# Optimization experiments

Measured on AMD Instinct MI355X. Metric: run time of the kernel, lower is better.

Reference implementation:

```python
import jax, jax.numpy as jnp
import numpy as np

N, S, T, E, H = 4, 2048, 2048, 512, 8
HD = E // H  # head_dim = 64


def setup_inputs() -> dict:
    key0 = jax.random.key(0)
    ks = jax.random.split(key0, 12)
    sc = 1.0 / np.sqrt(E)
    inp = {
        "query": jax.random.normal(ks[0], (N, S, E), jnp.float32),
        "key": jax.random.normal(ks[1], (N, T, E), jnp.float32),
        "value": jax.random.normal(ks[2], (N, T, E), jnp.float32),
        "attn_mask": jnp.tril(jnp.ones((S, T), jnp.int32)),  # causal: 0 => masked
        # nn.Linear weights (out, in) and biases, torch convention y = x @ W.T + b
        "Wq": jax.random.normal(ks[3], (E, E), jnp.float32) * sc,
        "bq": jax.random.normal(ks[4], (E,), jnp.float32) * sc,
        "Wk": jax.random.normal(ks[5], (E, E), jnp.float32) * sc,
        "bk": jax.random.normal(ks[6], (E,), jnp.float32) * sc,
        "Wv": jax.random.normal(ks[7], (E, E), jnp.float32) * sc,
        "bv": jax.random.normal(ks[8], (E,), jnp.float32) * sc,
        "Wp": jax.random.normal(ks[9], (E, E), jnp.float32) * sc,
        "bp": jax.random.normal(ks[10], (E,), jnp.float32) * sc,
    }
    return inp


def reference(query, key, value, attn_mask, Wq, bq, Wk, bk, Wv, bv, Wp, bp):
    # QKV projections, split heads: (N, H, L, HD)
    q = (query @ Wq.T + bq).reshape(N, S, H, HD).transpose(0, 2, 1, 3)
    k = (key @ Wk.T + bk).reshape(N, T, H, HD).transpose(0, 2, 1, 3)
    v = (value @ Wv.T + bv).reshape(N, T, H, HD).transpose(0, 2, 1, 3)
    # scaled scores (N, H, S, T) -- intentionally materialized like the original
    e = jnp.einsum("nhsd,nhtd->nhst", q, k) / jnp.sqrt(jnp.float32(HD))
    e = jnp.where(attn_mask == 0, -jnp.inf, e)
    a = jax.nn.softmax(e, axis=-1)
    # dropout is identity in eval mode (reference runs deterministic/eval)
    y = jnp.einsum("nhst,nhtd->nhsd", a, v)
    y = y.transpose(0, 2, 1, 3).reshape(N, S, E)
    return y @ Wp.T + bp
```

## Files before the change

kernel.cpp:

```cpp
#include <hip/hip_runtime.h>


#define DEV __device__ __forceinline__

typedef unsigned short u16;
typedef unsigned int u32;
typedef __bf16 bf16x8 __attribute__((ext_vector_type(8)));
typedef float f32x4 __attribute__((ext_vector_type(4)));

#define MFMA_BF16(A, B, C) __builtin_amdgcn_mfma_f32_16x16x32_bf16(A, B, C, 0, 0, 0)

DEV u16 f2bf(float f) {
  u32 u = __builtin_bit_cast(u32, f);
  u += 0x7fffu + ((u >> 16) & 1u);
  return (u16)(u >> 16);
}
DEV u16 f2bf_ru(float f) {
  u32 u = __builtin_bit_cast(u32, f);
  return (u16)((u + 0x8000u) >> 16);
}

DEV void cp16(void* l, const void* g) {
  __builtin_amdgcn_global_load_lds(
      (const __attribute__((address_space(1))) u32*)g,
      (__attribute__((address_space(3))) u32*)l, 16, 0, 0);
}

__global__ __launch_bounds__(256) void cast3(const float* __restrict__ q,
                                             const float* __restrict__ k,
                                             const float* __restrict__ v,
                                             u16* qo, u16* ko, u16* vo) {
  const float* s = (blockIdx.y == 0) ? q : (blockIdx.y == 1) ? k : v;
  u16* d = (blockIdx.y == 0) ? qo : (blockIdx.y == 1) ? ko : vo;
  int i = blockIdx.x * 256 + threadIdx.x;
  float4 f = ((const float4*)s)[i];
  ushort4 o;
  o.x = f2bf(f.x); o.y = f2bf(f.y); o.z = f2bf(f.z); o.w = f2bf(f.w);
  ((ushort4*)d)[i] = o;
}

__global__ __launch_bounds__(256) void cast4(const float* __restrict__ a,
                                             const float* __restrict__ b,
                                             const float* __restrict__ c,
                                             const float* __restrict__ d2,
                                             u16* ao, u16* bo, u16* co, u16* do_) {
  int y = blockIdx.y;
  const float* s = (y == 0) ? a : (y == 1) ? b : (y == 2) ? c : d2;
  u16* d = (y == 0) ? ao : (y == 1) ? bo : (y == 2) ? co : do_;
  int i = blockIdx.x * 256 + threadIdx.x;
  float4 f = ((const float4*)s)[i];
  ushort4 o;
  o.x = f2bf(f.x); o.y = f2bf(f.y); o.z = f2bf(f.z); o.w = f2bf(f.w);
  ((ushort4*)d)[i] = o;
}

DEV void gemm_loop(const u16* __restrict__ A, const u16* __restrict__ W,
                   u16* As, u16* Bs, int m0, int n0, int tid, f32x4 acc[4][4]) {
  const int lane = tid & 63, wid = tid >> 6;
  const int wm = wid & 1, wn = wid >> 1;
  const int l15 = lane & 15, l4 = lane >> 4;
  for (int kt = 0; kt < 512; kt += 32) {
    __syncthreads();
#pragma unroll
    for (int i = 0; i < 2; ++i) {
      int c = tid + 256 * i;
      int row = c >> 2, kc = (c & 3) * 8;
      cp16(&As[c * 8], A + (m0 + row) * 512 + kt + kc);
      cp16(&Bs[c * 8], W + (n0 + row) * 512 + kt + kc);
    }
    __syncthreads();
    bf16x8 af[4], bfr[4];
#pragma unroll
    for (int f = 0; f < 4; ++f) {
      af[f]  = *(const bf16x8*)&As[(wm * 64 + f * 16 + l15) * 32 + l4 * 8];
      bfr[f] = *(const bf16x8*)&Bs[(wn * 64 + f * 16 + l15) * 32 + l4 * 8];
    }
#pragma unroll
    for (int fm = 0; fm < 4; ++fm)
#pragma unroll
      for (int fn = 0; fn < 4; ++fn)
        acc[fm][fn] = MFMA_BF16(af[fm], bfr[fn], acc[fm][fn]);
  }
}

__global__ __launch_bounds__(256) void gemm_qkv(
    const u16* __restrict__ qx, const u16* __restrict__ kx, const u16* __restrict__ vx,
    const u16* __restrict__ wq, const u16* __restrict__ wk, const u16* __restrict__ wv,
    const float* __restrict__ bq, const float* __restrict__ bk, const float* __restrict__ bv,
    u16* qp, u16* kp, u16* vp) {
  __shared__ u16 As[128 * 32];
  __shared__ u16 Bs[128 * 32];
  const int wsel = blockIdx.x >> 2;
  const u16* A = (wsel == 0) ? qx : (wsel == 1) ? kx : vx;
  const u16* W = (wsel == 0) ? wq : (wsel == 1) ? wk : wv;
  const float* bias = (wsel == 0) ? bq : (wsel == 1) ? bk : bv;
  u16* C = (wsel == 0) ? qp : (wsel == 1) ? kp : vp;
  const int n0 = (blockIdx.x & 3) * 128, m0 = blockIdx.y * 128;
  const int tid = threadIdx.x, lane = tid & 63, wid = tid >> 6;
  const int wm = wid & 1, wn = wid >> 1;
  const int l15 = lane & 15, l4 = lane >> 4;

  f32x4 acc[4][4] = {};
  gemm_loop(A, W, As, Bs, m0, n0, tid, acc);

#pragma unroll
  for (int fn = 0; fn < 4; ++fn) {
    int col = n0 + wn * 64 + fn * 16 + l15;
    float bvv = bias[col];
#pragma unroll
    for (int fm = 0; fm < 4; ++fm) {
      int rowb = m0 + wm * 64 + fm * 16 + l4 * 4;
#pragma unroll
      for (int r = 0; r < 4; ++r)
        C[(rowb + r) * 512 + col] = f2bf(acc[fm][fn][r] + bvv);
    }
  }
}

__global__ __launch_bounds__(256) void gemm_out(const u16* __restrict__ A,
                                                const u16* __restrict__ W,
                                                const float* __restrict__ bias,
                                                float* __restrict__ C) {
  __shared__ u16 As[128 * 32];
  __shared__ u16 Bs[128 * 32];
  const int n0 = blockIdx.x * 128, m0 = blockIdx.y * 128;
  const int tid = threadIdx.x, lane = tid & 63, wid = tid >> 6;
  const int wm = wid & 1, wn = wid >> 1;
  const int l15 = lane & 15, l4 = lane >> 4;

  f32x4 acc[4][4] = {};
  gemm_loop(A, W, As, Bs, m0, n0, tid, acc);

#pragma unroll
  for (int fn = 0; fn < 4; ++fn) {
    int col = n0 + wn * 64 + fn * 16 + l15;
    float bvv = bias[col];
#pragma unroll
    for (int fm = 0; fm < 4; ++fm) {
      int rowb = m0 + wm * 64 + fm * 16 + l4 * 4;
#pragma unroll
      for (int r = 0; r < 4; ++r)
        C[(rowb + r) * 512 + col] = acc[fm][fn][r] + bvv;
    }
  }
}

__global__ __launch_bounds__(256) void transpose_v(const u16* __restrict__ vp,
                                                   u16* __restrict__ vt) {
  __shared__ u16 L[64 * 72];
  const int bid = blockIdx.x;
  const int nh = bid & 31, tt = bid >> 5;
  const int n = nh >> 3, h = nh & 7;
  const u16* src = vp + (n * 2048 + tt * 64) * 512 + h * 64;
  const int tid = threadIdx.x;
#pragma unroll
  for (int i = 0; i < 2; ++i) {
    int c = tid + 256 * i;
    int row = c >> 3, dg = c & 7;
    uint4 x = *(const uint4*)(src + row * 512 + dg * 8);
    *(uint4*)&L[row * 72 + dg * 8] = x;
  }
  __syncthreads();
  u16* dst = vt + nh * 64 * 2048 + tt * 64;
#pragma unroll
  for (int i = 0; i < 2; ++i) {
    int c = tid + 256 * i;
    int d = c >> 3, tg = c & 7;
    u16 e[8];
#pragma unroll
    for (int j = 0; j < 8; ++j) e[j] = L[(tg * 8 + j) * 72 + d];
    uint4 o;
    o.x = (u32)e[0] | ((u32)e[1] << 16);
    o.y = (u32)e[2] | ((u32)e[3] << 16);
    o.z = (u32)e[4] | ((u32)e[5] << 16);
    o.w = (u32)e[6] | ((u32)e[7] << 16);
    *(uint4*)(dst + d * 2048 + tg * 8) = o;
  }
}

__global__ __launch_bounds__(256) void attn_kernel(const u16* __restrict__ Qg,
                                                   const u16* __restrict__ Kg,
                                                   const u16* __restrict__ Vt,
                                                   u16* __restrict__ Yg) {
  __shared__ u16 Qs[64 * 64];
  __shared__ u16 KP[64 * 136];
  __shared__ u16 Vts[64 * 128];

  const int bid = blockIdx.x;
  const int nh = bid & 31;
  const int qt = 31 - (bid >> 5);
  const int n = nh >> 3, h = nh & 7;
  const int tid = threadIdx.x, lane = tid & 63, w = tid >> 6;
  const int l15 = lane & 15, l4 = lane >> 4;
  const int s0 = qt * 64;

  const u16* Qb = Qg + (n * 2048 + s0) * 512 + h * 64;
  const u16* Kb = Kg + n * 2048 * 512 + h * 64;
  const u16* Vb = Vt + nh * 64 * 2048;

#pragma unroll
  for (int i = 0; i < 2; ++i) {
    int c = tid + 256 * i;
    int row = c >> 3, dg = (c & 7) ^ (row & 7);
    cp16(&Qs[c * 8], Qb + row * 512 + dg * 8);
  }
  __syncthreads();
  const int qr = w * 16 + l15;
  bf16x8 qf0 = *(const bf16x8*)&Qs[qr * 64 + ((l4 ^ (qr & 7)) * 8)];
  bf16x8 qf1 = *(const bf16x8*)&Qs[qr * 64 + (((4 + l4) ^ (qr & 7)) * 8)];

  f32x4 accO[4] = {};
  float mrow = -1e30f, lrow = 0.f;
  const int sgl = s0 + w * 16 + l15;

  const int ntiles = (qt >> 1) + 1;
  for (int it = 0; it < ntiles; ++it) {
    const int t0 = it * 128;
    __syncthreads();
#pragma unroll
    for (int i = 0; i < 4; ++i) {
      int c = tid + 256 * i;
      int t = c >> 3, dg = (c & 7) ^ (t & 7);
      cp16(&KP[c * 8], Kb + (t0 + t) * 512 + dg * 8);
    }
#pragma unroll
    for (int i = 0; i < 4; ++i) {
      int c = tid + 256 * i;
      int d = c >> 4, tgs = c & 15;
      cp16(&Vts[c * 8], Vb + d * 2048 + t0 + ((tgs ^ (d & 15)) * 8));
    }
    __syncthreads();

    f32x4 st[8];
#pragma unroll
    for (int fn = 0; fn < 8; ++fn) {
      int tr = fn * 16 + l15;
      bf16x8 k0 = *(const bf16x8*)&KP[tr * 64 + ((l4 ^ (tr & 7)) * 8)];
      bf16x8 k1 = *(const bf16x8*)&KP[tr * 64 + (((4 + l4) ^ (tr & 7)) * 8)];
      f32x4 a = {};
      a = MFMA_BF16(k0, qf0, a);
      st[fn] = MFMA_BF16(k1, qf1, a);
    }

    const bool diag = (t0 + 128 > s0);
    const float SC = 0.18033688f;
    float rmax = -1e30f;
#pragma unroll
    for (int fn = 0; fn < 8; ++fn)
#pragma unroll
      for (int r = 0; r < 4; ++r) {
        float v = st[fn][r] * SC;
        if (diag) {
          int tg = t0 + fn * 16 + l4 * 4 + r;
          if (tg > sgl) v = -1e30f;
        }
        st[fn][r] = v;
        rmax = fmaxf(rmax, v);
      }
    rmax = fmaxf(rmax, __shfl_xor(rmax, 16));
    rmax = fmaxf(rmax, __shfl_xor(rmax, 32));
    float mnew = fmaxf(mrow, rmax);
    float alpha = __builtin_amdgcn_exp2f(mrow - mnew);
    mrow = mnew;
    float rsum = 0.f;
#pragma unroll
    for (int fn = 0; fn < 8; ++fn)
#pragma unroll
      for (int r = 0; r < 4; ++r) {
        float p = __builtin_amdgcn_exp2f(st[fn][r] - mnew);
        st[fn][r] = p;
        rsum += p;
      }
    rsum += __shfl_xor(rsum, 16);
    rsum += __shfl_xor(rsum, 32);
    lrow = lrow * alpha + rsum;

    float aO[4];
#pragma unroll
    for (int r = 0; r < 4; ++r) aO[r] = __shfl(alpha, (lane & 48) | (l4 * 4 + r));
#pragma unroll
    for (int fd = 0; fd < 4; ++fd)
#pragma unroll
      for (int r = 0; r < 4; ++r) accO[fd][r] *= aO[r];

    __syncthreads();

#pragma unroll
    for (int fn = 0; fn < 8; ++fn) {
      ushort4 pk;
      pk.x = f2bf_ru(st[fn][0]);
      pk.y = f2bf_ru(st[fn][1]);
      pk.z = f2bf_ru(st[fn][2]);
      pk.w = f2bf_ru(st[fn][3]);
      *(ushort4*)&KP[(w * 16 + l15) * 136 + fn * 16 + l4 * 4] = pk;
    }

#pragma unroll
    for (int ks = 0; ks < 4; ++ks) {
      bf16x8 ap = *(const bf16x8*)&KP[(w * 16 + l15) * 136 + ks * 32 + l4 * 8];
#pragma unroll
      for (int fd = 0; fd < 4; ++fd) {
        int d = fd * 16 + l15;
        bf16x8 bv = *(const bf16x8*)&Vts[d * 128 + (((ks * 4 + l4) ^ (d & 15)) * 8)];
        accO[fd] = MFMA_BF16(ap, bv, accO[fd]);
      }
    }
  }

  float lO[4];
#pragma unroll
  for (int r = 0; r < 4; ++r) lO[r] = __shfl(lrow, (lane & 48) | (l4 * 4 + r));
#pragma unroll
  for (int fd = 0; fd < 4; ++fd)
#pragma unroll
    for (int r = 0; r < 4; ++r) {
      int row = s0 + w * 16 + l4 * 4 + r;
      int col = h * 64 + fd * 16 + l15;
      Yg[(n * 2048 + row) * 512 + col] = f2bf(accO[fd][r] / lO[r]);
    }
}

extern "C" void kernel_launch(void* const* d_in, const int* in_sizes, int n_in,
                              void* d_out, int out_size, void* d_ws, size_t ws_size,
                              hipStream_t stream) {
  (void)in_sizes; (void)n_in; (void)out_size; (void)ws_size;
  const float* query = (const float*)d_in[0];
  const float* key_  = (const float*)d_in[1];
  const float* value = (const float*)d_in[2];
  const float* Wq = (const float*)d_in[4];
  const float* bq = (const float*)d_in[5];
  const float* Wk = (const float*)d_in[6];
  const float* bk = (const float*)d_in[7];
  const float* Wv = (const float*)d_in[8];
  const float* bv = (const float*)d_in[9];
  const float* Wp = (const float*)d_in[10];
  const float* bp = (const float*)d_in[11];

  char* ws = (char*)d_ws;
  u16* qx  = (u16*)(ws);
  u16* kx  = (u16*)(ws + 8388608);
  u16* vx  = (u16*)(ws + 16777216);
  u16* wqx = (u16*)(ws + 25165824);
  u16* wkx = (u16*)(ws + 25690112);
  u16* wvx = (u16*)(ws + 26214400);
  u16* wpx = (u16*)(ws + 26738688);
  u16* qp  = (u16*)(ws + 27262976);
  u16* kp  = (u16*)(ws + 35651584);
  u16* vp  = (u16*)(ws + 44040192);
  u16* y   = qx;
  u16* vt  = kx;

  cast3<<<dim3(4096, 3), 256, 0, stream>>>(query, key_, value, qx, kx, vx);
  cast4<<<dim3(256, 4), 256, 0, stream>>>(Wq, Wk, Wv, Wp, wqx, wkx, wvx, wpx);

  gemm_qkv<<<dim3(12, 64), 256, 0, stream>>>(qx, kx, vx, wqx, wkx, wvx,
                                             bq, bk, bv, qp, kp, vp);
  transpose_v<<<1024, 256, 0, stream>>>(vp, vt);
  attn_kernel<<<1024, 256, 0, stream>>>(qp, kp, vt, y);
  gemm_out<<<dim3(4, 64), 256, 0, stream>>>(y, wpx, bp, (float*)d_out);
}
```

Baseline: 209.0 us.

## Keep P in registers, fold softmax scale into Q, lazy rescale, retile out GEMM

Folds the softmax scale into the Q projection epilogue, removes the LDS round-trip for the probability tile by converting S accumulators directly into MFMA A operands with matching V reads, and skips the output rescale unless the running max grows by more than a threshold. It also adds s_setprio around MFMA blocks and halves the gemm_out M tile to double its grid. The aim is to cut LDS traffic, a barrier, and per-tile rescale ALU work, and to give the output GEMM more blocks. The lazy rescale lets exponentials exceed 1 by up to 2^10, which relies on fp32 and bf16 range.

```diff
diff --git a/kernel.cpp b/kernel.cpp
--- a/kernel.cpp
+++ b/kernel.cpp
@@ -7,6 +7,7 @@
 typedef unsigned int u32;
 typedef __bf16 bf16x8 __attribute__((ext_vector_type(8)));
 typedef float f32x4 __attribute__((ext_vector_type(4)));
+typedef u32 u32x4 __attribute__((ext_vector_type(4)));
 
 #define MFMA_BF16(A, B, C) __builtin_amdgcn_mfma_f32_16x16x32_bf16(A, B, C, 0, 0, 0)
 
@@ -14,10 +15,6 @@
   u32 u = __builtin_bit_cast(u32, f);
   u += 0x7fffu + ((u >> 16) & 1u);
   return (u16)(u >> 16);
-}
-DEV u16 f2bf_ru(float f) {
-  u32 u = __builtin_bit_cast(u32, f);
-  return (u16)((u + 0x8000u) >> 16);
 }
 
 DEV void cp16(void* l, const void* g) {
@@ -99,6 +96,7 @@
   const int tid = threadIdx.x, lane = tid & 63, wid = tid >> 6;
   const int wm = wid & 1, wn = wid >> 1;
   const int l15 = lane & 15, l4 = lane >> 4;
+  const float osc = (wsel == 0) ? 0.18033688f : 1.0f;
 
   f32x4 acc[4][4] = {};
   gemm_loop(A, W, As, Bs, m0, n0, tid, acc);
@@ -112,7 +110,7 @@
       int rowb = m0 + wm * 64 + fm * 16 + l4 * 4;
 #pragma unroll
       for (int r = 0; r < 4; ++r)
-        C[(rowb + r) * 512 + col] = f2bf(acc[fm][fn][r] + bvv);
+        C[(rowb + r) * 512 + col] = f2bf((acc[fm][fn][r] + bvv) * osc);
     }
   }
 }
@@ -121,23 +119,48 @@
                                                 const u16* __restrict__ W,
                                                 const float* __restrict__ bias,
                                                 float* __restrict__ C) {
-  __shared__ u16 As[128 * 32];
+  __shared__ u16 As[64 * 32];
   __shared__ u16 Bs[128 * 32];
-  const int n0 = blockIdx.x * 128, m0 = blockIdx.y * 128;
+  const int n0 = blockIdx.x * 128, m0 = blockIdx.y * 64;
   const int tid = threadIdx.x, lane = tid & 63, wid = tid >> 6;
   const int wm = wid & 1, wn = wid >> 1;
   const int l15 = lane & 15, l4 = lane >> 4;
 
-  f32x4 acc[4][4] = {};
-  gemm_loop(A, W, As, Bs, m0, n0, tid, acc);
+  f32x4 acc[2][4] = {};
+  for (int kt = 0; kt < 512; kt += 32) {
+    __syncthreads();
+    {
+      int row = tid >> 2, kc = (tid & 3) * 8;
+      cp16(&As[tid * 8], A + (m0 + row) * 512 + kt + kc);
+    }
+#pragma unroll
+    for (int i = 0; i < 2; ++i) {
+      int c = tid + 256 * i;
+      int row = c >> 2, kc = (c & 3) * 8;
+      cp16(&Bs[c * 8], W + (n0 + row) * 512 + kt + kc);
+    }
+    __syncthreads();
+    bf16x8 af[2], bfr[4];
+#pragma unroll
+    for (int f = 0; f < 2; ++f)
+      af[f] = *(const bf16x8*)&As[(wm * 32 + f * 16 + l15) * 32 + l4 * 8];
+#pragma unroll
+    for (int f = 0; f < 4; ++f)
+      bfr[f] = *(const bf16x8*)&Bs[(wn * 64 + f * 16 + l15) * 32 + l4 * 8];
+#pragma unroll
+    for (int fm = 0; fm < 2; ++fm)
+#pragma unroll
+      for (int fn = 0; fn < 4; ++fn)
+        acc[fm][fn] = MFMA_BF16(af[fm], bfr[fn], acc[fm][fn]);
+  }
 
 #pragma unroll
   for (int fn = 0; fn < 4; ++fn) {
     int col = n0 + wn * 64 + fn * 16 + l15;
     float bvv = bias[col];
 #pragma unroll
-    for (int fm = 0; fm < 4; ++fm) {
-      int rowb = m0 + wm * 64 + fm * 16 + l4 * 4;
+    for (int fm = 0; fm < 2; ++fm) {
+      int rowb = m0 + wm * 32 + fm * 16 + l4 * 4;
 #pragma unroll
       for (int r = 0; r < 4; ++r)
         C[(rowb + r) * 512 + col] = acc[fm][fn][r] + bvv;
@@ -183,7 +206,7 @@
                                                    const u16* __restrict__ Vt,
                                                    u16* __restrict__ Yg) {
   __shared__ u16 Qs[64 * 64];
-  __shared__ u16 KP[64 * 136];
+  __shared__ u16 Ks[128 * 64];
   __shared__ u16 Vts[64 * 128];
 
   const int bid = blockIdx.x;
@@ -221,7 +244,7 @@
     for (int i = 0; i < 4; ++i) {
       int c = tid + 256 * i;
       int t = c >> 3, dg = (c & 7) ^ (t & 7);
-      cp16(&KP[c * 8], Kb + (t0 + t) * 512 + dg * 8);
+      cp16(&Ks[c * 8], Kb + (t0 + t) * 512 + dg * 8);
     }
 #pragma unroll
     for (int i = 0; i < 4; ++i) {
@@ -232,24 +255,25 @@
     __syncthreads();
 
     f32x4 st[8];
+    __builtin_amdgcn_s_setprio(1);
 #pragma unroll
     for (int fn = 0; fn < 8; ++fn) {
       int tr = fn * 16 + l15;
-      bf16x8 k0 = *(const bf16x8*)&KP[tr * 64 + ((l4 ^ (tr & 7)) * 8)];
-      bf16x8 k1 = *(const bf16x8*)&KP[tr * 64 + (((4 + l4) ^ (tr & 7)) * 8)];
+      bf16x8 k0 = *(const bf16x8*)&Ks[tr * 64 + ((l4 ^ (tr & 7)) * 8)];
+      bf16x8 k1 = *(const bf16x8*)&Ks[tr * 64 + (((4 + l4) ^ (tr & 7)) * 8)];
       f32x4 a = {};
       a = MFMA_BF16(k0, qf0, a);
       st[fn] = MFMA_BF16(k1, qf1, a);
     }
+    __builtin_amdgcn_s_setprio(0);
 
     const bool diag = (t0 + 128 > s0);
-    const float SC = 0.18033688f;
     float rmax = -1e30f;
 #pragma unroll
     for (int fn = 0; fn < 8; ++fn)
 #pragma unroll
       for (int r = 0; r < 4; ++r) {
-        float v = st[fn][r] * SC;
+        float v = st[fn][r];
         if (diag) {
           int tg = t0 + fn * 16 + l4 * 4 + r;
           if (tg > sgl) v = -1e30f;
@@ -259,52 +283,57 @@
       }
     rmax = fmaxf(rmax, __shfl_xor(rmax, 16));
     rmax = fmaxf(rmax, __shfl_xor(rmax, 32));
-    float mnew = fmaxf(mrow, rmax);
-    float alpha = __builtin_amdgcn_exp2f(mrow - mnew);
-    mrow = mnew;
+    if (__any(rmax > mrow + 10.f)) {
+      float mnew = fmaxf(mrow, rmax);
+      float alpha = __builtin_amdgcn_exp2f(mrow - mnew);
+      mrow = mnew;
+      lrow *= alpha;
+      float aO[4];
+#pragma unroll
+      for (int r = 0; r < 4; ++r) aO[r] = __shfl(alpha, (lane & 48) | (l4 * 4 + r));
+#pragma unroll
+      for (int fd = 0; fd < 4; ++fd)
+#pragma unroll
+        for (int r = 0; r < 4; ++r) accO[fd][r] *= aO[r];
+    }
     float rsum = 0.f;
 #pragma unroll
     for (int fn = 0; fn < 8; ++fn)
 #pragma unroll
       for (int r = 0; r < 4; ++r) {
-        float p = __builtin_amdgcn_exp2f(st[fn][r] - mnew);
+        float p = __builtin_amdgcn_exp2f(st[fn][r] - mrow);
         st[fn][r] = p;
         rsum += p;
       }
     rsum += __shfl_xor(rsum, 16);
     rsum += __shfl_xor(rsum, 32);
-    lrow = lrow * alpha + rsum;
-
-    float aO[4];
-#pragma unroll
-    for (int r = 0; r < 4; ++r) aO[r] = __shfl(alpha, (lane & 48) | (l4 * 4 + r));
-#pragma unroll
-    for (int fd = 0; fd < 4; ++fd)
-#pragma unroll
-      for (int r = 0; r < 4; ++r) accO[fd][r] *= aO[r];
-
-    __syncthreads();
-
-#pragma unroll
-    for (int fn = 0; fn < 8; ++fn) {
-      ushort4 pk;
-      pk.x = f2bf_ru(st[fn][0]);
-      pk.y = f2bf_ru(st[fn][1]);
-      pk.z = f2bf_ru(st[fn][2]);
-      pk.w = f2bf_ru(st[fn][3]);
-      *(ushort4*)&KP[(w * 16 + l15) * 136 + fn * 16 + l4 * 4] = pk;
-    }
-
+    lrow += rsum;
+
+    bf16x8 pa[4];
 #pragma unroll
     for (int ks = 0; ks < 4; ++ks) {
-      bf16x8 ap = *(const bf16x8*)&KP[(w * 16 + l15) * 136 + ks * 32 + l4 * 8];
+      bf16x8 t;
+      t[0] = (__bf16)st[2 * ks][0];     t[1] = (__bf16)st[2 * ks][1];
+      t[2] = (__bf16)st[2 * ks][2];     t[3] = (__bf16)st[2 * ks][3];
+      t[4] = (__bf16)st[2 * ks + 1][0]; t[5] = (__bf16)st[2 * ks + 1][1];
+      t[6] = (__bf16)st[2 * ks + 1][2]; t[7] = (__bf16)st[2 * ks + 1][3];
+      pa[ks] = t;
+    }
+
+    __builtin_amdgcn_s_setprio(1);
+#pragma unroll
+    for (int ks = 0; ks < 4; ++ks) {
 #pragma unroll
       for (int fd = 0; fd < 4; ++fd) {
         int d = fd * 16 + l15;
-        bf16x8 bv = *(const bf16x8*)&Vts[d * 128 + (((ks * 4 + l4) ^ (d & 15)) * 8)];
-        accO[fd] = MFMA_BF16(ap, bv, accO[fd]);
+        const u16* vrow = &Vts[d * 128];
+        uint2 v0 = *(const uint2*)&vrow[(((ks * 4 + (l4 >> 1)) ^ l15) * 8) + (l4 & 1) * 4];
+        uint2 v1 = *(const uint2*)&vrow[(((ks * 4 + 2 + (l4 >> 1)) ^ l15) * 8) + (l4 & 1) * 4];
+        u32x4 bw; bw.x = v0.x; bw.y = v0.y; bw.z = v1.x; bw.w = v1.y;
+        accO[fd] = MFMA_BF16(pa[ks], __builtin_bit_cast(bf16x8, bw), accO[fd]);
       }
     }
+    __builtin_amdgcn_s_setprio(0);
   }
 
   float lO[4];
@@ -357,5 +386,5 @@
                                              bq, bk, bv, qp, kp, vp);
   transpose_v<<<1024, 256, 0, stream>>>(vp, vt);
   attn_kernel<<<1024, 256, 0, stream>>>(qp, kp, vt, y);
-  gemm_out<<<dim3(4, 64), 256, 0, stream>>>(y, wpx, bp, (float*)d_out);
-}
+  gemm_out<<<dim3(4, 128), 256, 0, stream>>>(y, wpx, bp, (float*)d_out);
+}
```

After: 204.1 us. 2.3% less time.
